# Performance work log

Measured on AMD Instinct MI355X. Metric: run time of the kernel, lower is better.

The kernel has to match this reference:

```python
import jax, jax.numpy as jnp
import numpy as np

NUM_GROUPS = 32
EPS = 1e-6


def group_norm(x, gamma, beta):
    # x: [B, C, H, W]; GroupNorm over (channels-in-group, H, W)
    B, C, H, W = x.shape
    xg = x.reshape(B, NUM_GROUPS, C // NUM_GROUPS, H, W)
    mean = xg.mean(axis=(2, 3, 4), keepdims=True)
    var = xg.var(axis=(2, 3, 4), keepdims=True)
    xn = ((xg - mean) * jax.lax.rsqrt(var + EPS)).reshape(B, C, H, W)
    return xn * gamma[None, :, None, None] + beta[None, :, None, None]


def conv1x1(x, w, b):
    # 1x1 conv == channel-mixing matmul. w: [C_out, C_in]
    return jnp.einsum('bchw,oc->bohw', x, w) + b[None, :, None, None]


def setup_inputs() -> dict:
    key = jax.random.key(0)
    ks = jax.random.split(key, 6)
    B, C, H, W = 8, 256, 64, 64
    s = 1.0 / np.sqrt(C)  # fan-in scaled weights (like Conv2d default)
    inp = {
        'x': jax.random.normal(ks[0], (B, C, H, W), jnp.float32),
        'gamma': jnp.ones((C,), jnp.float32),
        'beta': jnp.zeros((C,), jnp.float32),
        'wq': jax.random.normal(ks[1], (C, C), jnp.float32) * s,
        'bq': jnp.zeros((C,), jnp.float32),
        'wk': jax.random.normal(ks[2], (C, C), jnp.float32) * s,
        'bk': jnp.zeros((C,), jnp.float32),
        'wv': jax.random.normal(ks[3], (C, C), jnp.float32) * s,
        'bv': jnp.zeros((C,), jnp.float32),
        'wo': jax.random.normal(ks[4], (C, C), jnp.float32) * s,
        'bo': jnp.zeros((C,), jnp.float32),
    }
    return inp


def reference(x, gamma, beta, wq, bq, wk, bk, wv, bv, wo, bo):
    B, C, H, W = x.shape
    h = group_norm(x, gamma, beta)
    q = conv1x1(h, wq, bq)
    k = conv1x1(h, wk, bk)
    v = conv1x1(h, wv, bv)
    # elu + 1 feature map (nonnegative kernel features)
    q = jax.nn.elu(q) + 1.0
    k = jax.nn.elu(k) + 1.0
    N = H * W
    kf = k.reshape(B, C, N)            # [B, C, N]
    vf = v.reshape(B, C, N)            # [B, C, N]
    qf = q.reshape(B, C, N)            # [B, C, N]
    # kv = k @ v^T : [B, C, C]
    kv = jnp.einsum('bcn,bdn->bcd', kf, vf)
    # h_out[b, n, d] = sum_c q[b, c, n] * kv[b, c, d]; stored channel-first
    h_out = jnp.einsum('bcn,bcd->bdn', qf, kv).reshape(B, C, H, W)
    return x + conv1x1(h_out, wo, bo)
```

## Files before the change

kernel.cpp:

```cpp
#include <hip/hip_runtime.h>
#include <math.h>

#define C_DIM 256
#define N_DIM 4096
#define B_DIM 8

typedef __attribute__((ext_vector_type(8))) short bf16x8;
typedef __attribute__((ext_vector_type(4))) float f32x4;
typedef __attribute__((ext_vector_type(8))) unsigned short us8;
typedef __attribute__((ext_vector_type(4))) unsigned short us4;

__device__ inline unsigned short f2bf(float f) {
    unsigned int u = __float_as_uint(f);
    u += 0x7fffu + ((u >> 16) & 1u);
    return (unsigned short)(u >> 16);
}

__device__ inline void gload_lds16(const void* g, void* l) {
    __builtin_amdgcn_global_load_lds(
        (const __attribute__((address_space(1))) unsigned int*)g,
        (__attribute__((address_space(3))) unsigned int*)l, 16, 0, 0);
}

__global__ __launch_bounds__(256) void prep_kernel(
    const float* __restrict__ wq, const float* __restrict__ wk,
    const float* __restrict__ wv, const float* __restrict__ wo,
    const float* __restrict__ bk, const float* __restrict__ bv,
    const float* __restrict__ x,
    unsigned short* __restrict__ wqb, unsigned short* __restrict__ wkvb,
    unsigned short* __restrict__ wob, float* __restrict__ bkv,
    float2* __restrict__ sums)
{
    int z = blockIdx.x;
    int t = threadIdx.x;
    if (z < 256) {
        const float* s; unsigned short* d;
        int which = z >> 6;
        if (which == 0)      { s = wq; d = wqb; }
        else if (which == 1) { s = wk; d = wkvb; }
        else if (which == 2) { s = wv; d = wkvb + 65536; }
        else                 { s = wo; d = wob; }
        int idx = (z & 63) * 1024 + t * 4;
        float4 v = *(const float4*)(s + idx);
        us4 r; r[0] = f2bf(v.x); r[1] = f2bf(v.y); r[2] = f2bf(v.z); r[3] = f2bf(v.w);
        *(us4*)(d + idx) = r;
    } else if (z == 256) {
        bkv[t]       = bk[t];
        bkv[t + 256] = bv[t];
    } else {
        int bc = z - 257;
        const float* xc = x + (size_t)bc * N_DIM;
        float s = 0.f, q = 0.f;
        for (int i = t; i < 1024; i += 256) {
            float4 v = ((const float4*)xc)[i];
            s += v.x + v.y + v.z + v.w;
            q += v.x*v.x + v.y*v.y + v.z*v.z + v.w*v.w;
        }
        #pragma unroll
        for (int off = 32; off > 0; off >>= 1) {
            s += __shfl_down(s, off);
            q += __shfl_down(q, off);
        }
        __shared__ float red[8];
        int w = t >> 6;
        if ((t & 63) == 0) { red[w*2] = s; red[w*2+1] = q; }
        __syncthreads();
        if (t == 0) {
            sums[bc] = make_float2(red[0]+red[2]+red[4]+red[6],
                                   red[1]+red[3]+red[5]+red[7]);
        }
    }
}

__global__ __launch_bounds__(256) void gn_apply(const float* __restrict__ x,
                                                const float2* __restrict__ sums,
                                                const float* __restrict__ gamma,
                                                const float* __restrict__ beta,
                                                unsigned short* __restrict__ hT) {
    int b = blockIdx.y, n0 = blockIdx.x * 64;
    int t = threadIdx.x;
    __shared__ float scale[256], shift[256];
    __shared__ unsigned short trans[64][264];

    {
        int c = t;
        int gbase = c & ~7;
        float s = 0.f, q = 0.f;
        #pragma unroll
        for (int j = 0; j < 8; j++) {
            float2 u = sums[b*256 + gbase + j];
            s += u.x; q += u.y;
        }
        float mean = s * (1.f/32768.f);
        float var  = q * (1.f/32768.f) - mean*mean;
        float inv  = rsqrtf(var + 1e-6f);
        float gm = gamma[c] * inv;
        scale[c] = gm;
        shift[c] = beta[c] - mean * gm;
    }
    __syncthreads();

    #pragma unroll
    for (int it = 0; it < 16; it++) {
        int c  = it*16 + (t >> 4);
        int nl = (t & 15) * 4;
        float4 v = *(const float4*)(x + ((size_t)(b*C_DIM + c))*N_DIM + n0 + nl);
        float sc = scale[c], sh = shift[c];
        trans[nl+0][c] = f2bf(v.x*sc + sh);
        trans[nl+1][c] = f2bf(v.y*sc + sh);
        trans[nl+2][c] = f2bf(v.z*sc + sh);
        trans[nl+3][c] = f2bf(v.w*sc + sh);
    }
    __syncthreads();

    #pragma unroll
    for (int it = 0; it < 8; it++) {
        int nl = it*8 + (t >> 5);
        int cb = (t & 31) * 8;
        us8 vv = *(us8*)&trans[nl][cb];
        *(us8*)(hT + ((size_t)b*N_DIM + n0 + nl)*C_DIM + cb) = vv;
    }
}

__global__ __launch_bounds__(256) void kvred(const float* __restrict__ src, unsigned short* __restrict__ dst) {
    int gi = (blockIdx.x * 256 + threadIdx.x) * 4;
    int b = gi >> 16, idx = gi & 65535;
    float4 a = make_float4(0.f,0.f,0.f,0.f);
    #pragma unroll
    for (int sp = 0; sp < 8; sp++) {
        float4 v = *(const float4*)(src + (((size_t)b*8 + sp) << 16) + idx);
        a.x += v.x; a.y += v.y; a.z += v.z; a.w += v.w;
    }
    us4 r; r[0] = f2bf(a.x); r[1] = f2bf(a.y); r[2] = f2bf(a.z); r[3] = f2bf(a.w);
    *(us4*)(dst + ((size_t)b << 16) + idx) = r;
}

template<int MODE>
__device__ __forceinline__ void gemm_body(
    const unsigned short* __restrict__ Ab, const unsigned short* __restrict__ Bb,
    const float* __restrict__ bias, const float* __restrict__ residb,
    void* __restrict__ Cb,
    int N, int K, int k0, int Ks, int m_blk, int n_blk, bool elu,
    char* smem)
{
    unsigned short* lds = (unsigned short*)smem;

    int t = threadIdx.x;
    int w = t >> 6, l = t & 63;
    int wm = w >> 1, wn = w & 1;
    int l15 = l & 15, quad = l >> 4;

    int srow = w * 16 + (l >> 2);
    int skc  = (((l & 3) ^ ((l >> 3) & 3)) * 8);

    f32x4 acc[4][4];
    #pragma unroll
    for (int i = 0; i < 4; i++)
        #pragma unroll
        for (int j = 0; j < 4; j++)
            #pragma unroll
            for (int r = 0; r < 4; r++) acc[i][j][r] = 0.f;

    auto stage = [&](int buf, int kt) {
        unsigned short* Asl = lds + buf*8192 + t*8;
        unsigned short* Bsl = Asl + 4096;
        #pragma unroll
        for (int rep = 0; rep < 2; rep++) {
            gload_lds16(Ab + (size_t)(m_blk + rep*64 + srow) * K + kt + skc, Asl + rep*2048);
            gload_lds16(Bb + (size_t)(n_blk + rep*64 + srow) * K + kt + skc, Bsl + rep*2048);
        }
    };

    const int nt = Ks >> 5;

    stage(0, k0);
    if (nt > 1) stage(1, k0 + 32);

    int rsw = (l15 >> 1) & 3;
    int acol = (quad ^ rsw) * 8;

    int bufc = 0;
    for (int kt = 0; kt < nt; ++kt) {
        if (kt + 1 < nt) asm volatile("s_waitcnt vmcnt(4)" ::: "memory");
        else             asm volatile("s_waitcnt vmcnt(0)" ::: "memory");
        __builtin_amdgcn_s_barrier();
        __builtin_amdgcn_sched_barrier(0);
        if (kt + 2 < nt) {
            int bufn = bufc + 2; if (bufn >= 3) bufn -= 3;
            stage(bufn, k0 + (kt + 2) * 32);
        }
        __builtin_amdgcn_sched_barrier(0);

        const unsigned short* Aw = lds + bufc*8192 + (wm*64 + l15)*32 + acol;
        const unsigned short* Bw = lds + bufc*8192 + 4096 + (wn*64 + l15)*32 + acol;
        bf16x8 af[4], bfr[4];
        #pragma unroll
        for (int i = 0; i < 4; i++) af[i]  = *(const bf16x8*)(Aw + i*512);
        #pragma unroll
        for (int j = 0; j < 4; j++) bfr[j] = *(const bf16x8*)(Bw + j*512);
        __builtin_amdgcn_s_setprio(1);
        #pragma unroll
        for (int i = 0; i < 4; i++)
            #pragma unroll
            for (int j = 0; j < 4; j++)
                acc[i][j] = __builtin_amdgcn_mfma_f32_16x16x32_bf16(af[i], bfr[j], acc[i][j], 0, 0, 0);
        __builtin_amdgcn_s_setprio(0);
        bufc = (bufc == 2) ? 0 : bufc + 1;
    }
    __syncthreads();

    if (MODE == 0 || MODE == 1 || MODE == 4) {
        unsigned short* ep = (unsigned short*)smem;
        unsigned short* Cp = (unsigned short*)Cb;
        #pragma unroll
        for (int h = 0; h < 2; h++) {
            if (wm == h) {
                int row0 = quad*4;
                int col0 = wn*64 + l15;
                #pragma unroll
                for (int i = 0; i < 4; i++) {
                    #pragma unroll
                    for (int j = 0; j < 4; j++) {
                        int cl = col0 + j*16;
                        #pragma unroll
                        for (int r = 0; r < 4; r++) {
                            int rl = row0 + i*16 + r;
                            float val = acc[i][j][r];
                            if (MODE == 0) {
                                val += bias[n_blk + cl];
                                val = val > 0.f ? val + 1.f : __expf(val);
                            } else if (MODE == 1) {
                                val += bias[m_blk + h*64 + rl];
                                if (elu) val = val > 0.f ? val + 1.f : __expf(val);
                            }
                            ep[rl*136 + cl] = f2bf(val);
                        }
                    }
                }
            }
            __syncthreads();
            #pragma unroll
            for (int it = 0; it < 4; it++) {
                int row = it*16 + (t >> 4);
                int col = (t & 15) * 8;
                us8 vv = *(us8*)(ep + row*136 + col);
                *(us8*)(Cp + (size_t)(m_blk + h*64 + row) * N + n_blk + col) = vv;
            }
            __syncthreads();
        }
    } else {
        float* ep32 = (float*)smem;
        float* Cp = (float*)Cb;
        #pragma unroll
        for (int h = 0; h < 2; h++) {
            if (wm == h) {
                int row0 = quad*4;
                int col0 = wn*64 + l15;
                #pragma unroll
                for (int i = 0; i < 4; i++)
                    #pragma unroll
                    for (int j = 0; j < 4; j++)
                        #pragma unroll
                        for (int r = 0; r < 4; r++)
                            ep32[(row0 + i*16 + r)*140 + col0 + j*16] = acc[i][j][r];
            }
            __syncthreads();
            #pragma unroll
            for (int it = 0; it < 8; it++) {
                int rl  = it*8 + (t >> 5);
                int row = m_blk + h*64 + rl;
                int col = (t & 31) * 4;
                f32x4 vv = *(f32x4*)(ep32 + rl*140 + col);
                if (MODE == 5) {
                    float bi = bias[row];
                    float4 rv = *(const float4*)(residb + (size_t)row * N + n_blk + col);
                    vv[0] += bi + rv.x; vv[1] += bi + rv.y;
                    vv[2] += bi + rv.z; vv[3] += bi + rv.w;
                }
                *(f32x4*)(Cp + (size_t)row * N + n_blk + col) = vv;
            }
            __syncthreads();
        }
    }
}

__global__ __launch_bounds__(256) void qkv_kernel(
    const unsigned short* __restrict__ hT, const unsigned short* __restrict__ wqb,
    const unsigned short* __restrict__ wkvb,
    const float* __restrict__ bq, const float* __restrict__ bkv,
    unsigned short* __restrict__ qT, unsigned short* __restrict__ kvbuf)
{
    __shared__ __align__(16) char smem[49152];
    int z = blockIdx.x;
    if (z < 512) {
        int b = z >> 6, rem = z & 63;
        int m_blk = (rem >> 1) * 128, n_blk = (rem & 1) * 128;
        gemm_body<0>(hT + (size_t)b*1048576, wqb, bq, nullptr,
                     qT + (size_t)b*1048576,
                     256, 256, 0, 256, m_blk, n_blk, true, smem);
    } else {
        int iz = z - 512;
        int b = iz >> 7, rem = iz & 127;
        int m_blk = (rem >> 5) * 128, n_blk = (rem & 31) * 128;
        gemm_body<1>(wkvb, hT + (size_t)b*1048576, bkv, nullptr,
                     kvbuf + (size_t)b*2097152,
                     4096, 256, 0, 256, m_blk, n_blk, m_blk < 256, smem);
    }
}

template<int MODE>
__global__ __launch_bounds__(256) void gemm_nt(
    const unsigned short* __restrict__ A, const unsigned short* __restrict__ B,
    const float* __restrict__ bias, const float* __restrict__ resid,
    void* __restrict__ Cout,
    int N, int K, int splits,
    size_t sA, size_t sB, size_t sC, size_t sR, int elem4)
{
    __shared__ __align__(16) char smem[49152];
    int b  = blockIdx.z / splits;
    int sp = blockIdx.z % splits;
    int Ks = K / splits;
    size_t cbase = (MODE == 3) ? ((size_t)(b*splits + sp)) * sC : (size_t)b * sC;
    void* Cb = elem4 ? (void*)((float*)Cout + cbase) : (void*)((unsigned short*)Cout + cbase);
    gemm_body<MODE>(A + b*sA, B + b*sB, bias,
                    resid ? resid + b*sR : nullptr, Cb,
                    N, K, sp*Ks, Ks, blockIdx.y*128, blockIdx.x*128, false, smem);
}

extern "C" void kernel_launch(void* const* d_in, const int* in_sizes, int n_in,
                              void* d_out, int out_size, void* d_ws, size_t ws_size,
                              hipStream_t stream) {
    const float* x     = (const float*)d_in[0];
    const float* gamma = (const float*)d_in[1];
    const float* beta  = (const float*)d_in[2];
    const float* wq    = (const float*)d_in[3];
    const float* bq    = (const float*)d_in[4];
    const float* wk    = (const float*)d_in[5];
    const float* bk    = (const float*)d_in[6];
    const float* wv    = (const float*)d_in[7];
    const float* bv    = (const float*)d_in[8];
    const float* wo    = (const float*)d_in[9];
    const float* bo    = (const float*)d_in[10];
    float* out = (float*)d_out;

    const size_t TEN = (size_t)B_DIM * C_DIM * N_DIM;
    unsigned short* ws16  = (unsigned short*)d_ws;
    unsigned short* hT    = ws16;
    unsigned short* qT    = hT    + TEN;
    unsigned short* kvbuf = qT    + TEN;
    unsigned short* kvb   = kvbuf + 2*TEN;
    unsigned short* M2b   = kvb   + 524288;
    unsigned short* wqb   = M2b   + 524288;
    unsigned short* wkvb  = wqb   + 65536;
    unsigned short* wob   = wkvb  + 131072;
    float*          bkv   = (float*)(wob + 65536);
    float2*         sums  = (float2*)(bkv + 512);
    float*          kvf   = (float*)(sums + 2048);

    prep_kernel<<<dim3(2305), 256, 0, stream>>>(wq, wk, wv, wo, bk, bv, x,
                                                wqb, wkvb, wob, bkv, sums);
    gn_apply<<<dim3(N_DIM/64, B_DIM), 256, 0, stream>>>(x, sums, gamma, beta, hT);
    qkv_kernel<<<dim3(1536), 256, 0, stream>>>(hT, wqb, wkvb, bq, bkv, qT, kvbuf);
    gemm_nt<3><<<dim3(2, 2, B_DIM*8), 256, 0, stream>>>(
        kvbuf, kvbuf + 1048576, nullptr, nullptr, kvf,
        256, 4096, 8, 2097152, 2097152, 65536, 0, 1);
    kvred<<<dim3(512), 256, 0, stream>>>(kvf, kvb);
    gemm_nt<4><<<dim3(2, 2, B_DIM), 256, 0, stream>>>(
        wob, kvb, nullptr, nullptr, M2b,
        256, 256, 1, 0, 65536, 65536, 0, 0);
    gemm_nt<5><<<dim3(32, 2, B_DIM), 256, 0, stream>>>(
        M2b, qT, bo, x, out,
        4096, 256, 1, 65536, 1048576, 1048576, 1048576, 1);
}
```

Before: 182.6 us.

## Use 128x256 tiles for QKV projection GEMM to halve block count

Replaces the QKV projection kernel with a templated GEMM using 128x256 (or 256x128) output tiles, so each block covers the full 256-wide output dimension and re-reads of the activation tile are halved. The grid drops from 1536 to 768 blocks with larger LDS (72KB) and launch_bounds(256,2). The epilogue is rewritten for the larger tiles. The cost is more accumulator registers per thread and lower occupancy.

```diff
diff --git a/kernel.cpp b/kernel.cpp
--- a/kernel.cpp
+++ b/kernel.cpp
@@ -135,13 +135,178 @@
     *(us4*)(dst + ((size_t)b << 16) + idx) = r;
 }
 
+template<int RI, int RJ, int MODE>
+__device__ __forceinline__ void gemm2_body(
+    const unsigned short* __restrict__ Ab,
+    const unsigned short* __restrict__ Bb,
+    const float* __restrict__ bias,
+    unsigned short* __restrict__ Cp,
+    int crow0, int ccol0, bool elu, char* smem)
+{
+    constexpr int M = RI * 32, N = RJ * 32;
+    constexpr int ACH = M / 64;
+    constexpr int BCH = N / 64;
+    unsigned short* lds = (unsigned short*)smem;
+
+    int t = threadIdx.x;
+    int w = t >> 6, l = t & 63;
+    int wm = w >> 1, wn = w & 1;
+    int l15 = l & 15, quad = l >> 4;
+
+    f32x4 acc[RI][RJ];
+    #pragma unroll
+    for (int i = 0; i < RI; i++)
+        #pragma unroll
+        for (int j = 0; j < RJ; j++)
+            #pragma unroll
+            for (int r = 0; r < 4; r++) acc[i][j][r] = 0.f;
+
+    auto stage = [&](int buf, int kt) {
+        unsigned short* Ls = lds + buf * (M*32 + N*32);
+        #pragma unroll
+        for (int s = 0; s < ACH; s++) {
+            int c = t + s*256, row = c >> 2;
+            int cs = (c & 3) ^ ((row >> 1) & 3);
+            gload_lds16(Ab + (size_t)row*256 + kt + cs*8, Ls + c*8);
+        }
+        #pragma unroll
+        for (int s = 0; s < BCH; s++) {
+            int c = t + s*256, row = c >> 2;
+            int cs = (c & 3) ^ ((row >> 1) & 3);
+            gload_lds16(Bb + (size_t)row*256 + kt + cs*8, Ls + M*32 + c*8);
+        }
+    };
+
+    stage(0, 0);
+    stage(1, 32);
+
+    int acol = (quad ^ ((l15 >> 1) & 3)) * 8;
+
+    int bufc = 0;
+    for (int kt = 0; kt < 8; ++kt) {
+        if (kt + 1 < 8) asm volatile("s_waitcnt vmcnt(6)" ::: "memory");
+        else            asm volatile("s_waitcnt vmcnt(0)" ::: "memory");
+        __builtin_amdgcn_s_barrier();
+        __builtin_amdgcn_sched_barrier(0);
+        if (kt + 2 < 8) {
+            int bufn = bufc + 2; if (bufn >= 3) bufn -= 3;
+            stage(bufn, (kt + 2) * 32);
+        }
+        __builtin_amdgcn_sched_barrier(0);
+
+        const unsigned short* As = lds + bufc * (M*32 + N*32);
+        const unsigned short* Bs = As + M*32;
+        bf16x8 af[RI], bfr[RJ];
+        #pragma unroll
+        for (int i = 0; i < RI; i++)
+            af[i]  = *(const bf16x8*)(As + (wm*(RI*16) + i*16 + l15)*32 + acol);
+        #pragma unroll
+        for (int j = 0; j < RJ; j++)
+            bfr[j] = *(const bf16x8*)(Bs + (wn*(RJ*16) + j*16 + l15)*32 + acol);
+        __builtin_amdgcn_s_setprio(1);
+        #pragma unroll
+        for (int i = 0; i < RI; i++)
+            #pragma unroll
+            for (int j = 0; j < RJ; j++)
+                acc[i][j] = __builtin_amdgcn_mfma_f32_16x16x32_bf16(af[i], bfr[j], acc[i][j], 0, 0, 0);
+        __builtin_amdgcn_s_setprio(0);
+        bufc = (bufc == 2) ? 0 : bufc + 1;
+    }
+    __syncthreads();
+
+    if (MODE == 0) {
+        unsigned short* ep = (unsigned short*)smem;
+        #pragma unroll
+        for (int h = 0; h < 2; h++) {
+            if (wm == h) {
+                #pragma unroll
+                for (int i = 0; i < RI; i++) {
+                    #pragma unroll
+                    for (int j = 0; j < RJ; j++) {
+                        int cl = wn*128 + j*16 + l15;
+                        float bi = bias[cl];
+                        #pragma unroll
+                        for (int r = 0; r < 4; r++) {
+                            int rl = quad*4 + i*16 + r;
+                            float val = acc[i][j][r] + bi;
+                            val = val > 0.f ? val + 1.f : __expf(val);
+                            ep[rl*264 + cl] = f2bf(val);
+                        }
+                    }
+                }
+            }
+            __syncthreads();
+            #pragma unroll
+            for (int it = 0; it < 8; it++) {
+                int row = it*8 + (t >> 5);
+                int colc = (t & 31) * 8;
+                us8 vv = *(us8*)(ep + row*264 + colc);
+                *(us8*)(Cp + (size_t)(crow0 + h*64 + row)*256 + colc) = vv;
+            }
+            __syncthreads();
+        }
+    } else {
+        unsigned short* ep = (unsigned short*)smem;
+        #pragma unroll
+        for (int h = 0; h < 2; h++) {
+            if (wm == h) {
+                #pragma unroll
+                for (int i = 0; i < RI; i++) {
+                    #pragma unroll
+                    for (int j = 0; j < RJ; j++) {
+                        int cl = wn*64 + j*16 + l15;
+                        #pragma unroll
+                        for (int r = 0; r < 4; r++) {
+                            int rl = quad*4 + i*16 + r;
+                            float val = acc[i][j][r] + bias[crow0 + h*128 + rl];
+                            if (elu) val = val > 0.f ? val + 1.f : __expf(val);
+                            ep[rl*136 + cl] = f2bf(val);
+                        }
+                    }
+                }
+            }
+            __syncthreads();
+            #pragma unroll
+            for (int it = 0; it < 8; it++) {
+                int row = it*16 + (t >> 4);
+                int colc = (t & 15) * 8;
+                us8 vv = *(us8*)(ep + row*136 + colc);
+                *(us8*)(Cp + (size_t)(crow0 + h*128 + row)*4096 + ccol0 + colc) = vv;
+            }
+            __syncthreads();
+        }
+    }
+}
+
+__global__ __launch_bounds__(256, 2) void qkv2(
+    const unsigned short* __restrict__ hT, const unsigned short* __restrict__ wqb,
+    const unsigned short* __restrict__ wkvb,
+    const float* __restrict__ bq, const float* __restrict__ bkv,
+    unsigned short* __restrict__ qT, unsigned short* __restrict__ kvbuf)
+{
+    __shared__ __align__(16) char smem[73728];
+    int z = blockIdx.x;
+    if (z < 256) {
+        int b = z >> 5, m_blk = (z & 31) * 128;
+        gemm2_body<4,8,0>(hT + (size_t)b*1048576 + (size_t)m_blk*256, wqb,
+                          bq, qT + (size_t)b*1048576, m_blk, 0, true, smem);
+    } else {
+        int iz = z - 256;
+        int b = iz >> 6, rem = iz & 63;
+        int mh = rem >> 5, n_blk = (rem & 31) * 128;
+        gemm2_body<8,4,1>(wkvb + (size_t)mh*65536,
+                          hT + (size_t)b*1048576 + (size_t)n_blk*256,
+                          bkv, kvbuf + (size_t)b*2097152,
+                          mh*256, n_blk, mh == 0, smem);
+    }
+}
+
 template<int MODE>
 __device__ __forceinline__ void gemm_body(
     const unsigned short* __restrict__ Ab, const unsigned short* __restrict__ Bb,
     const float* __restrict__ bias, const float* __restrict__ residb,
     void* __restrict__ Cb,
-    int N, int K, int k0, int Ks, int m_blk, int n_blk, bool elu,
-    char* smem)
+    int N, int K, int k0, int Ks, int m_blk, int n_blk, char* smem)
 {
     unsigned short* lds = (unsigned short*)smem;
 
@@ -176,8 +341,7 @@
     stage(0, k0);
     if (nt > 1) stage(1, k0 + 32);
 
-    int rsw = (l15 >> 1) & 3;
-    int acol = (quad ^ rsw) * 8;
+    int acol = (quad ^ ((l15 >> 1) & 3)) * 8;
 
     int bufc = 0;
     for (int kt = 0; kt < nt; ++kt) {
@@ -209,7 +373,7 @@
     }
     __syncthreads();
 
-    if (MODE == 0 || MODE == 1 || MODE == 4) {
+    if (MODE == 4) {
         unsigned short* ep = (unsigned short*)smem;
         unsigned short* Cp = (unsigned short*)Cb;
         #pragma unroll
@@ -218,25 +382,12 @@
                 int row0 = quad*4;
                 int col0 = wn*64 + l15;
                 #pragma unroll
-                for (int i = 0; i < 4; i++) {
+                for (int i = 0; i < 4; i++)
                     #pragma unroll
-                    for (int j = 0; j < 4; j++) {
-                        int cl = col0 + j*16;
+                    for (int j = 0; j < 4; j++)
                         #pragma unroll
-                        for (int r = 0; r < 4; r++) {
-                            int rl = row0 + i*16 + r;
-                            float val = acc[i][j][r];
-                            if (MODE == 0) {
-                                val += bias[n_blk + cl];
-                                val = val > 0.f ? val + 1.f : __expf(val);
-                            } else if (MODE == 1) {
-                                val += bias[m_blk + h*64 + rl];
-                                if (elu) val = val > 0.f ? val + 1.f : __expf(val);
-                            }
-                            ep[rl*136 + cl] = f2bf(val);
-                        }
-                    }
-                }
+                        for (int r = 0; r < 4; r++)
+                            ep[(row0 + i*16 + r)*136 + col0 + j*16] = f2bf(acc[i][j][r]);
             }
             __syncthreads();
             #pragma unroll
@@ -281,30 +432,6 @@
             }
             __syncthreads();
         }
-    }
-}
-
-__global__ __launch_bounds__(256) void qkv_kernel(
-    const unsigned short* __restrict__ hT, const unsigned short* __restrict__ wqb,
-    const unsigned short* __restrict__ wkvb,
-    const float* __restrict__ bq, const float* __restrict__ bkv,
-    unsigned short* __restrict__ qT, unsigned short* __restrict__ kvbuf)
-{
-    __shared__ __align__(16) char smem[49152];
-    int z = blockIdx.x;
-    if (z < 512) {
-        int b = z >> 6, rem = z & 63;
-        int m_blk = (rem >> 1) * 128, n_blk = (rem & 1) * 128;
-        gemm_body<0>(hT + (size_t)b*1048576, wqb, bq, nullptr,
-                     qT + (size_t)b*1048576,
-                     256, 256, 0, 256, m_blk, n_blk, true, smem);
-    } else {
-        int iz = z - 512;
-        int b = iz >> 7, rem = iz & 127;
-        int m_blk = (rem >> 5) * 128, n_blk = (rem & 31) * 128;
-        gemm_body<1>(wkvb, hT + (size_t)b*1048576, bkv, nullptr,
-                     kvbuf + (size_t)b*2097152,
-                     4096, 256, 0, 256, m_blk, n_blk, m_blk < 256, smem);
     }
 }
 
@@ -324,7 +451,7 @@
     void* Cb = elem4 ? (void*)((float*)Cout + cbase) : (void*)((unsigned short*)Cout + cbase);
     gemm_body<MODE>(A + b*sA, B + b*sB, bias,
                     resid ? resid + b*sR : nullptr, Cb,
-                    N, K, sp*Ks, Ks, blockIdx.y*128, blockIdx.x*128, false, smem);
+                    N, K, sp*Ks, Ks, blockIdx.y*128, blockIdx.x*128, smem);
 }
 
 extern "C" void kernel_launch(void* const* d_in, const int* in_sizes, int n_in,
@@ -360,7 +487,7 @@
     prep_kernel<<<dim3(2305), 256, 0, stream>>>(wq, wk, wv, wo, bk, bv, x,
                                                 wqb, wkvb, wob, bkv, sums);
     gn_apply<<<dim3(N_DIM/64, B_DIM), 256, 0, stream>>>(x, sums, gamma, beta, hT);
-    qkv_kernel<<<dim3(1536), 256, 0, stream>>>(hT, wqb, wkvb, bq, bkv, qT, kvbuf);
+    qkv2<<<dim3(768), 256, 0, stream>>>(hT, wqb, wkvb, bq, bkv, qT, kvbuf);
     gemm_nt<3><<<dim3(2, 2, B_DIM*8), 256, 0, stream>>>(
         kvbuf, kvbuf + 1048576, nullptr, nullptr, kvf,
         256, 4096, 8, 2097152, 2097152, 65536, 0, 1);
```

Result: no change. 186.1 us (+1.9%).
